# Optimization experiments

Hardware: AMD Instinct MI355X
Metric: run time of the kernel (lower is better)

## Reference

```python
import jax, jax.numpy as jnp
import numpy as np

DIM = 128
N_CENTERS = 30
CUT_LO, CUT_HI = 0.0, 10.0
N_CONV = 3
NODE_VOCAB = 100
EDGE_VOCAB = 500
N_NODES = 50000
N_EDGES = 800000
N_GRAPHS = 100
DIM_E = DIM + N_CENTERS  # 158


def setup_inputs() -> dict:
    key = jax.random.key(0)
    ks = jax.random.split(key, 20)
    def xav(k, shape):
        fan_in = shape[-2] if len(shape) >= 2 else shape[-1]
        return (jax.random.normal(k, shape, dtype=jnp.float32) / np.sqrt(fan_in)).astype(jnp.float32)
    inp = {
        'node_types': jax.random.randint(ks[0], (N_NODES,), 0, NODE_VOCAB),
        'edge_types': jax.random.randint(ks[1], (N_EDGES,), 0, EDGE_VOCAB),
        'src': jax.random.randint(ks[2], (N_EDGES,), 0, N_NODES),
        'dst': jax.random.randint(ks[3], (N_EDGES,), 0, N_NODES),
        'graph_ids': jnp.sort(jax.random.randint(ks[4], (N_NODES,), 0, N_GRAPHS)),
        'distances': jax.random.uniform(ks[5], (N_EDGES,), dtype=jnp.float32, minval=CUT_LO, maxval=CUT_HI),
        'n_graphs': N_GRAPHS,
        # embedding tables
        'node_emb': xav(ks[6], (NODE_VOCAB, DIM)),
        'edge_emb': xav(ks[7], (EDGE_VOCAB, DIM)),
        # stacked per-conv-layer weights (n_conv leading dim)
        'Wn1': xav(ks[8], (N_CONV, DIM, DIM)),  'bn1': jnp.zeros((N_CONV, DIM), jnp.float32),
        'Wn2': xav(ks[9], (N_CONV, DIM, DIM)),  'bn2': jnp.zeros((N_CONV, DIM), jnp.float32),
        'We1': xav(ks[10], (N_CONV, DIM_E, DIM)), 'be1': jnp.zeros((N_CONV, DIM), jnp.float32),
        'We2': xav(ks[11], (N_CONV, DIM, DIM)),  'be2': jnp.zeros((N_CONV, DIM), jnp.float32),
        'Wc':  xav(ks[12], (N_CONV, DIM, DIM)),  'bc': jnp.zeros((N_CONV, DIM), jnp.float32),
        # read layer
        'Wr1': xav(ks[13], (DIM, DIM)), 'br1': jnp.zeros((DIM,), jnp.float32),
        'Wr2': xav(ks[14], (DIM, 1)),   'br2': jnp.zeros((1,), jnp.float32),
    }
    return inp


def reference(node_types, edge_types, src, dst, graph_ids, distances, n_graphs,
              node_emb, edge_emb, Wn1, bn1, Wn2, bn2, We1, be1, We2, be2, Wc, bc,
              Wr1, br1, Wr2, br2):
    # embeddings
    h = node_emb[node_types]                      # [N, D]
    e_emb = edge_emb[edge_types]                  # [E, D]
    # RBF expansion of distances
    centers = jnp.linspace(CUT_LO, CUT_HI, N_CENTERS, dtype=jnp.float32)
    gap = centers[1] - centers[0]
    rbf = jnp.exp(-((distances[:, None] - centers[None, :]) ** 2) / gap)  # [E, n_centers]
    e = jnp.concatenate([e_emb, rbf], axis=1)     # [E, D + n_centers]

    n_nodes = h.shape[0]
    for i in range(N_CONV):
        node_path = jnp.maximum(h[src] @ Wn1[i] + bn1[i], 0.0) @ Wn2[i] + bn2[i]   # [E, D]
        edge_path = jnp.maximum(e @ We1[i] + be1[i], 0.0) @ We2[i] + be2[i]        # [E, D]
        m = jnp.tanh((node_path * edge_path) @ Wc[i] + bc[i])                       # [E, D]
        h = h + jax.ops.segment_sum(m, dst, num_segments=n_nodes)                   # scatter-add to dst

    # readout MLP + per-graph node sum
    hr = jnp.maximum(h @ Wr1 + br1, 0.0) @ Wr2 + br2                                # [N, 1]
    out = jax.ops.segment_sum(hr, graph_ids, num_segments=n_graphs)                 # [G, 1]
    return out.reshape(-1)
```

## Files before the change

kernel.cpp:

```cpp
#include <hip/hip_runtime.h>
#include <stdint.h>

#define NNODES 50000
#define NEDGES 800000
#define NGRAPH 100
#define NCHUNK (NEDGES / 16)
#define NWAVES 4096
#define NB0 196

typedef _Float16 f16;
typedef __attribute__((ext_vector_type(8))) _Float16 half8;
typedef __attribute__((ext_vector_type(4))) _Float16 half4;
typedef __attribute__((ext_vector_type(4))) float floatx4;

__device__ __forceinline__ void stage_WT(const float* __restrict__ W, f16* WT,
                                         int tid, int nthr) {
    for (int idx = tid; idx < 128 * 32; idx += nthr) {
        int k = idx >> 5, n4 = (idx & 31) * 4;
        floatx4 v = *(const floatx4*)(W + k * 128 + n4);
        WT[(n4 + 0) * 136 + k] = (f16)v[0];
        WT[(n4 + 1) * 136 + k] = (f16)v[1];
        WT[(n4 + 2) * 136 + k] = (f16)v[2];
        WT[(n4 + 3) * 136 + k] = (f16)v[3];
    }
}

__device__ __forceinline__ float fast_tanh(float x) {
    x = fminf(fmaxf(x, -15.0f), 15.0f);
    float e2 = __expf(2.0f * x);
    return (e2 - 1.0f) * __builtin_amdgcn_rcpf(e2 + 1.0f);
}

__device__ __forceinline__ int mtAddr(int c, int rgroup) {
    return c * 16 + ((((c >> 2) + rgroup) & 3) << 2);
}

__global__ void init_k(float* out, int osz, int* cnt) {
    int i = blockIdx.x * 256 + threadIdx.x;
    if (i < osz) out[i] = 0.0f;
    if (i < NNODES) cnt[i] = 0;
}

__global__ void hist_k(const int* __restrict__ dst, int* __restrict__ cnt) {
    int e = blockIdx.x * 256 + threadIdx.x;
    if (e < NEDGES) atomicAdd(&cnt[dst[e]], 1);
}

__global__ __launch_bounds__(1024) void scan1_k(const int* __restrict__ cnt,
                                                int* __restrict__ rowStart,
                                                int* __restrict__ blockSum) {
    __shared__ int buf[1024];
    int tid = threadIdx.x;
    int i = blockIdx.x * 1024 + tid;
    int v = (i < NNODES) ? cnt[i] : 0;
    buf[tid] = v;
    __syncthreads();
    for (int off = 1; off < 1024; off <<= 1) {
        int t = (tid >= off) ? buf[tid - off] : 0;
        __syncthreads();
        buf[tid] += t;
        __syncthreads();
    }
    if (i < NNODES) rowStart[i] = buf[tid] - v;
    if (tid == 1023) blockSum[blockIdx.x] = buf[1023];
}

__global__ void scan2_k(int* __restrict__ blockSum, int nb) {
    if (threadIdx.x == 0) {
        int run = 0;
        for (int b = 0; b < nb; ++b) { int s = blockSum[b]; blockSum[b] = run; run += s; }
    }
}

__global__ __launch_bounds__(1024) void scan3_k(int* __restrict__ rowStart,
                                                const int* __restrict__ blockSum,
                                                int* __restrict__ cnt) {
    int i = blockIdx.x * 1024 + threadIdx.x;
    if (i < NNODES) { rowStart[i] += blockSum[blockIdx.x]; cnt[i] = 0; }
    if (i == 0) rowStart[NNODES] = NEDGES;
}

__global__ void scatter_k(const int* __restrict__ src, const int* __restrict__ et,
                          const int* __restrict__ dst, const float* __restrict__ dist,
                          const int* __restrict__ rowStart, int* __restrict__ cnt,
                          uint4* __restrict__ packE) {
    int e = blockIdx.x * 256 + threadIdx.x;
    if (e >= NEDGES) return;
    int d = dst[e];
    int pos = rowStart[d] + atomicAdd(&cnt[d], 1);
    uint4 pk;
    pk.x = (unsigned)src[e];
    pk.y = (unsigned)et[e];
    pk.z = (unsigned)d;
    pk.w = __float_as_uint(dist[e]);
    packE[pos] = pk;
}

__global__ void gather_h(const int* __restrict__ nt, const float* __restrict__ emb,
                         float* __restrict__ h) {
    int i = blockIdx.x * 256 + threadIdx.x;
    int row = i >> 5, c4 = (i & 31) * 4;
    if (row < NNODES)
        *(floatx4*)(h + row * 128 + c4) = *(const floatx4*)(emb + nt[row] * 128 + c4);
}

__global__ __launch_bounds__(1024, 4) void mlp_combo(
        const float* __restrict__ Xh,
        const float* __restrict__ W1, const float* __restrict__ b1,
        const float* __restrict__ W2, const float* __restrict__ b2,
        f16* __restrict__ OutP,
        const float* __restrict__ Xe,
        const float* __restrict__ We1, const float* __restrict__ be1,
        f16* __restrict__ OutT) {
    __shared__ f16 W1T[128 * 136];
    __shared__ f16 W2T[128 * 136];
    __shared__ f16 xBuf[256 * 136];
    __shared__ float bias1[128];
    __shared__ float bias2[128];
    int tid = threadIdx.x;
    bool mode2 = blockIdx.x >= NB0;

    const float* X  = mode2 ? Xe : Xh;
    const float* Wa = mode2 ? We1 : W1;
    const float* ba = mode2 ? be1 : b1;
    f16* Out        = mode2 ? OutT : OutP;
    int  M          = mode2 ? 500 : NNODES;
    int  r0         = (mode2 ? (blockIdx.x - NB0) : blockIdx.x) * 256;

    stage_WT(Wa, W1T, tid, 1024);
    if (!mode2) stage_WT(W2, W2T, tid, 1024);
    if (tid < 128) { bias1[tid] = ba[tid]; bias2[tid] = mode2 ? 0.0f : b2[tid]; }

    for (int it = 0; it < 8; ++it) {
        int row = it * 32 + (tid >> 5);
        int c4 = (tid & 31) * 4;
        int gr = r0 + row;
        floatx4 x = {0.0f, 0.0f, 0.0f, 0.0f};
        if (gr < M) x = *(const floatx4*)(X + (size_t)gr * 128 + c4);
        half4 xh;
        xh[0] = (f16)x[0]; xh[1] = (f16)x[1]; xh[2] = (f16)x[2]; xh[3] = (f16)x[3];
        *(half4*)(xBuf + row * 136 + c4) = xh;
    }
    __syncthreads();

    int lane = tid & 63, wv = tid >> 6;
    int R = wv * 16;
    int n16 = lane & 15, q = lane >> 4;
    int gr = r0 + R + n16;

    half8 a[4];
    #pragma unroll
    for (int kk = 0; kk < 4; ++kk)
        a[kk] = *(const half8*)(xBuf + (R + n16) * 136 + kk * 32 + q * 8);

    #pragma unroll
    for (int f = 0; f < 8; ++f) {
        floatx4 acc = *(const floatx4*)(bias1 + f * 16 + q * 4);
        #pragma unroll
        for (int kk = 0; kk < 4; ++kk) {
            half8 aw = *(const half8*)(W1T + (f * 16 + n16) * 136 + kk * 32 + q * 8);
            acc = __builtin_amdgcn_mfma_f32_16x16x32_f16(aw, a[kk], acc, 0, 0, 0);
        }
        if (!mode2) {
            half4 y;
            #pragma unroll
            for (int i = 0; i < 4; ++i) y[i] = (f16)fmaxf(acc[i], 0.0f);
            *(half4*)(xBuf + (R + n16) * 136 + f * 16 + q * 4) = y;
        } else {
            half4 o;
            #pragma unroll
            for (int i = 0; i < 4; ++i) o[i] = (f16)acc[i];
            if (gr < M) *(half4*)(Out + (size_t)gr * 128 + f * 16 + q * 4) = o;
        }
    }

    if (!mode2) {
        #pragma unroll
        for (int kk = 0; kk < 4; ++kk)
            a[kk] = *(const half8*)(xBuf + (R + n16) * 136 + kk * 32 + q * 8);
        #pragma unroll
        for (int f = 0; f < 8; ++f) {
            floatx4 acc = *(const floatx4*)(bias2 + f * 16 + q * 4);
            #pragma unroll
            for (int kk = 0; kk < 4; ++kk) {
                half8 aw = *(const half8*)(W2T + (f * 16 + n16) * 136 + kk * 32 + q * 8);
                acc = __builtin_amdgcn_mfma_f32_16x16x32_f16(aw, a[kk], acc, 0, 0, 0);
            }
            half4 o;
            #pragma unroll
            for (int i = 0; i < 4; ++i) o[i] = (f16)acc[i];
            if (gr < M) *(half4*)(Out + (size_t)gr * 128 + f * 16 + q * 4) = o;
        }
    }
}

__global__ __launch_bounds__(1024, 4) void edge_kernel(
        const uint4* __restrict__ packE,
        const f16* __restrict__ P, const f16* __restrict__ T,
        const float* __restrict__ We1,
        const float* __restrict__ We2, const float* __restrict__ be2,
        const float* __restrict__ Wc,  const float* __restrict__ bc,
        float* __restrict__ h) {
    __shared__ f16 W2T[128 * 136];
    __shared__ f16 WcT[128 * 136];
    __shared__ f16 W1rT[128 * 40];
    __shared__ f16 Uall[16 * 2176];
    __shared__ float sbe2[128], sbc[128];
    __shared__ int dstW[16][16];

    int tid = threadIdx.x;
    stage_WT(We2, W2T, tid, 1024);
    stage_WT(Wc,  WcT, tid, 1024);
    for (int idx = tid; idx < 128 * 32; idx += 1024) {
        int n = idx >> 5, kr = idx & 31;
        W1rT[n * 40 + kr] = (kr < 30) ? (f16)We1[(128 + kr) * 128 + n] : (f16)0.0f;
    }
    if (tid < 128) { sbe2[tid] = be2[tid]; sbc[tid] = bc[tid]; }
    __syncthreads();

    int lane = tid & 63, wv = tid >> 6;
    f16* U = Uall + wv * 2176;
    int* dW = dstW[wv];
    int n16 = lane & 15, q = lane >> 4;
    const float invgap = 29.0f / 10.0f;
    int colA = lane, colB = lane + 64;
    int tsub = lane & 3, trow = lane >> 2;

    float sbcv[8];
    #pragma unroll
    for (int f = 0; f < 8; ++f) sbcv[f] = sbc[f * 16 + n16];

    int wgid = blockIdx.x * 16 + wv;
    int extra = wgid < 848 ? wgid : 848;
    int c0 = wgid * 12 + extra;
    int c1 = c0 + 12 + (wgid < 848 ? 1 : 0);

    float carry0 = 0.0f, carry1 = 0.0f;
    int prev = -1;

    uint4 pk = {0u, 0u, 0u, 0u};
    if (lane < 16) pk = packE[(size_t)c0 * 16 + lane];

    for (int ch = c0; ch < c1; ++ch) {
        bool hasNext = (ch + 1 < c1);
        int   ety  = __shfl((int)pk.y, trow);
        int   srcv = __shfl((int)pk.x, n16);
        float dcur = __shfl(__uint_as_float(pk.w), n16);
        if (lane < 16) dW[lane] = (int)pk.z;

        {
            const uint4* Tp = (const uint4*)(T + (size_t)ety * 128 + tsub * 32);
            uint4 tr0 = Tp[0], tr1 = Tp[1], tr2 = Tp[2], tr3 = Tp[3];
            uint4* ub = (uint4*)(U + trow * 136 + tsub * 32);
            ub[0] = tr0; ub[1] = tr1; ub[2] = tr2; ub[3] = tr3;
        }
        __builtin_amdgcn_sched_barrier(0);

        half8 pA0, pA1, pA2, pA3;
        {
            const f16* Pr = P + (size_t)srcv * 128 + q * 8;
            pA0 = *(const half8*)(Pr);
            pA1 = *(const half8*)(Pr + 32);
            pA2 = *(const half8*)(Pr + 64);
            pA3 = *(const half8*)(Pr + 96);
        }
        uint4 pkn = {0u, 0u, 0u, 0u};
        if (hasNext && lane < 16) pkn = packE[(size_t)(ch + 1) * 16 + lane];

        half8 ar;
        #pragma unroll
        for (int j = 0; j < 8; ++j) {
            int k = q * 8 + j;
            float c = (float)k * (10.0f / 29.0f);
            float df = dcur - c;
            ar[j] = (f16)((k < 30) ? __expf(-df * df * invgap) : 0.0f);
        }

        #pragma unroll
        for (int f = 0; f < 8; ++f) {
            f16* up = U + n16 * 136 + f * 16 + q * 4;
            half4 tv = *(const half4*)up;
            floatx4 c4 = {(float)tv[0], (float)tv[1], (float)tv[2], (float)tv[3]};
            half8 aw = *(const half8*)(W1rT + (f * 16 + n16) * 40 + q * 8);
            c4 = __builtin_amdgcn_mfma_f32_16x16x32_f16(aw, ar, c4, 0, 0, 0);
            half4 uv;
            #pragma unroll
            for (int i = 0; i < 4; ++i) uv[i] = (f16)fmaxf(c4[i], 0.0f);
            *(half4*)up = uv;
        }

        half8 a2[4];
        #pragma unroll
        for (int kk = 0; kk < 4; ++kk)
            a2[kk] = *(const half8*)(U + n16 * 136 + kk * 32 + q * 8);
        #pragma unroll
        for (int f = 0; f < 8; ++f) {
            floatx4 acc = *(const floatx4*)(sbe2 + f * 16 + q * 4);
            #pragma unroll
            for (int kk = 0; kk < 4; ++kk) {
                half8 aw = *(const half8*)(W2T + (f * 16 + n16) * 136 + kk * 32 + q * 8);
                acc = __builtin_amdgcn_mfma_f32_16x16x32_f16(aw, a2[kk], acc, 0, 0, 0);
            }
            half4 ev;
            #pragma unroll
            for (int i = 0; i < 4; ++i) ev[i] = (f16)acc[i];
            *(half4*)(U + n16 * 136 + f * 16 + q * 4) = ev;
        }

        {
            half8 e0 = *(const half8*)(U + n16 * 136 + 0 * 32 + q * 8);
            half8 e1 = *(const half8*)(U + n16 * 136 + 1 * 32 + q * 8);
            half8 e2 = *(const half8*)(U + n16 * 136 + 2 * 32 + q * 8);
            half8 e3 = *(const half8*)(U + n16 * 136 + 3 * 32 + q * 8);
            a2[0] = e0 * pA0; a2[1] = e1 * pA1; a2[2] = e2 * pA2; a2[3] = e3 * pA3;
        }
        #pragma unroll
        for (int f = 0; f < 8; ++f) {
            float bb = sbcv[f];
            floatx4 acc = {bb, bb, bb, bb};
            #pragma unroll
            for (int kk = 0; kk < 4; ++kk) {
                half8 b = *(const half8*)(WcT + (f * 16 + n16) * 136 + kk * 32 + q * 8);
                acc = __builtin_amdgcn_mfma_f32_16x16x32_f16(a2[kk], b, acc, 0, 0, 0);
            }
            int c = f * 16 + n16;
            half4 mv;
            #pragma unroll
            for (int i = 0; i < 4; ++i) mv[i] = (f16)fast_tanh(acc[i]);
            *(half4*)(U + mtAddr(c, q)) = mv;
        }

        {
            half4 va[4], vb[4];
            #pragma unroll
            for (int g2 = 0; g2 < 4; ++g2) {
                va[g2] = *(const half4*)(U + mtAddr(colA, g2));
                vb[g2] = *(const half4*)(U + mtAddr(colB, g2));
            }
            int dArr[16];
            *(int4*)(dArr)      = *(const int4*)(dW);
            *(int4*)(dArr + 4)  = *(const int4*)(dW + 4);
            *(int4*)(dArr + 8)  = *(const int4*)(dW + 8);
            *(int4*)(dArr + 12) = *(const int4*)(dW + 12);
            #pragma unroll
            for (int r = 0; r < 16; ++r) {
                int dd = dArr[r];
                float v0 = (float)va[r >> 2][r & 3];
                float v1 = (float)vb[r >> 2][r & 3];
                if (dd != prev) {
                    if (prev >= 0) {
                        unsafeAtomicAdd(&h[(size_t)prev * 128 + colA], carry0);
                        unsafeAtomicAdd(&h[(size_t)prev * 128 + colB], carry1);
                    }
                    prev = dd; carry0 = v0; carry1 = v1;
                } else { carry0 += v0; carry1 += v1; }
            }
        }
        pk = pkn;
        __builtin_amdgcn_sched_barrier(0);
    }
    if (prev >= 0) {
        unsafeAtomicAdd(&h[(size_t)prev * 128 + colA], carry0);
        unsafeAtomicAdd(&h[(size_t)prev * 128 + colB], carry1);
    }
}

__global__ __launch_bounds__(1024, 4) void readout_k(
        const float* __restrict__ X, int M,
        const float* __restrict__ W1, const float* __restrict__ b1,
        const float* __restrict__ Wr2, const float* __restrict__ br2,
        const int* __restrict__ gid, float* __restrict__ out) {
    __shared__ f16 W1T[128 * 136];
    __shared__ f16 xBuf[256 * 136];
    __shared__ float bias1[128];
    __shared__ float sWr2[128];
    int tid = threadIdx.x;

    stage_WT(W1, W1T, tid, 1024);
    if (tid < 128) { bias1[tid] = b1[tid]; sWr2[tid] = Wr2[tid]; }

    int r0 = blockIdx.x * 256;
    for (int it = 0; it < 8; ++it) {
        int row = it * 32 + (tid >> 5);
        int c4 = (tid & 31) * 4;
        int gr = r0 + row;
        floatx4 x = {0.0f, 0.0f, 0.0f, 0.0f};
        if (gr < M) x = *(const floatx4*)(X + (size_t)gr * 128 + c4);
        half4 xh;
        xh[0] = (f16)x[0]; xh[1] = (f16)x[1]; xh[2] = (f16)x[2]; xh[3] = (f16)x[3];
        *(half4*)(xBuf + row * 136 + c4) = xh;
    }
    __syncthreads();

    int lane = tid & 63, wv = tid >> 6;
    int R = wv * 16;
    int n16 = lane & 15, q = lane >> 4;

    half8 a[4];
    #pragma unroll
    for (int kk = 0; kk < 4; ++kk)
        a[kk] = *(const half8*)(xBuf + (R + n16) * 136 + kk * 32 + q * 8);

    floatx4 acc[8];
    #pragma unroll
    for (int f = 0; f < 8; ++f) {
        float bb = bias1[f * 16 + n16];
        acc[f] = (floatx4){bb, bb, bb, bb};
        #pragma unroll
        for (int kk = 0; kk < 4; ++kk) {
            half8 b = *(const half8*)(W1T + (f * 16 + n16) * 136 + kk * 32 + q * 8);
            acc[f] = __builtin_amdgcn_mfma_f32_16x16x32_f16(a[kk], b, acc[f], 0, 0, 0);
        }
    }

    float s[4];
    #pragma unroll
    for (int i = 0; i < 4; ++i) {
        float t = 0.0f;
        #pragma unroll
        for (int f = 0; f < 8; ++f)
            t += fmaxf(acc[f][i], 0.0f) * sWr2[f * 16 + n16];
        #pragma unroll
        for (int m = 1; m < 16; m <<= 1) t += __shfl_xor(t, m);
        s[i] = t;
    }

    if (n16 == 0) {
        float br2v = br2[0];
        float t = 0.0f; int g = -1;
        #pragma unroll
        for (int i = 0; i < 4; ++i) {
            int gr = r0 + R + q * 4 + i;
            if (gr < M) {
                int gi = gid[gr];
                float si = s[i] + br2v;
                if (gi == g) t += si;
                else { if (g >= 0) unsafeAtomicAdd(&out[g], t); g = gi; t = si; }
            }
        }
        if (g >= 0) unsafeAtomicAdd(&out[g], t);
    }
}

extern "C" void kernel_launch(void* const* d_in, const int* in_sizes, int n_in,
                              void* d_out, int out_size, void* d_ws, size_t ws_size,
                              hipStream_t stream) {
    (void)in_sizes; (void)n_in; (void)ws_size;
    const int*   node_types = (const int*)d_in[0];
    const int*   edge_types = (const int*)d_in[1];
    const int*   src        = (const int*)d_in[2];
    const int*   dst        = (const int*)d_in[3];
    const int*   graph_ids  = (const int*)d_in[4];
    const float* distances  = (const float*)d_in[5];
    const float* node_emb   = (const float*)d_in[7];
    const float* edge_emb   = (const float*)d_in[8];
    const float* Wn1 = (const float*)d_in[9];
    const float* bn1 = (const float*)d_in[10];
    const float* Wn2 = (const float*)d_in[11];
    const float* bn2 = (const float*)d_in[12];
    const float* We1 = (const float*)d_in[13];
    const float* be1 = (const float*)d_in[14];
    const float* We2 = (const float*)d_in[15];
    const float* be2 = (const float*)d_in[16];
    const float* Wc  = (const float*)d_in[17];
    const float* bc  = (const float*)d_in[18];
    const float* Wr1 = (const float*)d_in[19];
    const float* br1 = (const float*)d_in[20];
    const float* Wr2 = (const float*)d_in[21];
    const float* br2 = (const float*)d_in[22];

    char* w = (char*)d_ws;
    auto carve = [&](size_t bytes) { char* p = w; w += (bytes + 255) & ~(size_t)255; return p; };
    float* h        = (float*)carve((size_t)NNODES * 128 * 4);
    f16*   P        = (f16*)  carve((size_t)NNODES * 128 * 2);
    f16*   T        = (f16*)  carve((size_t)500 * 128 * 2);
    int*   rowStart = (int*)  carve((size_t)(NNODES + 1) * 4);
    int*   cnt      = (int*)  carve((size_t)NNODES * 4);
    int*   blockSum = (int*)  carve((size_t)64 * 4);
    uint4* packE    = (uint4*)carve((size_t)NEDGES * 16);

    float* out = (float*)d_out;
    const int NB1 = (NNODES + 1023) / 1024;

    init_k<<<(NNODES + 255) / 256, 256, 0, stream>>>(out, out_size, cnt);
    hist_k<<<NEDGES / 256, 256, 0, stream>>>(dst, cnt);
    scan1_k<<<NB1, 1024, 0, stream>>>(cnt, rowStart, blockSum);
    scan2_k<<<1, 64, 0, stream>>>(blockSum, NB1);
    scan3_k<<<NB1, 1024, 0, stream>>>(rowStart, blockSum, cnt);
    scatter_k<<<NEDGES / 256, 256, 0, stream>>>(src, edge_types, dst, distances,
                                                rowStart, cnt, packE);
    gather_h<<<(NNODES * 32 + 255) / 256, 256, 0, stream>>>(node_types, node_emb, h);

    for (int i = 0; i < 3; ++i) {
        mlp_combo<<<NB0 + 2, 1024, 0, stream>>>(
            h, Wn1 + (size_t)i * 128 * 128, bn1 + i * 128,
            Wn2 + (size_t)i * 128 * 128, bn2 + i * 128, P,
            edge_emb, We1 + (size_t)i * 158 * 128, be1 + i * 128, T);
        edge_kernel<<<256, 1024, 0, stream>>>(
            packE, P, T,
            We1 + (size_t)i * 158 * 128,
            We2 + (size_t)i * 128 * 128, be2 + i * 128,
            Wc + (size_t)i * 128 * 128, bc + i * 128, h);
    }

    readout_k<<<(NNODES + 255) / 256, 1024, 0, stream>>>(
        h, NNODES, Wr1, br1, Wr2, br2, graph_ids, out);
}
```

Measured before the change: 686.5 us.

## Replace per-edge RBF expansion and matmul with a quantized distance lookup table

A new kernel precomputes, for each layer, the RBF-expansion-times-We1 product for 4096 distance bins over the cutoff range and stores it in fp16. The scatter pass stores a bin index instead of the raw distance. The edge kernel then adds the looked-up row to the edge-type row and applies ReLU, which removes the per-edge exp evaluations and the RBF MFMA stage. It also simplifies tanh by dropping the clamp and moves the biases into registers. In exchange it adds an extra table gather per edge and quantization error, and distances outside the cutoff range are clamped to the edge bins.

```diff
diff --git a/kernel.cpp b/kernel.cpp
--- a/kernel.cpp
+++ b/kernel.cpp
@@ -7,6 +7,7 @@
 #define NCHUNK (NEDGES / 16)
 #define NWAVES 4096
 #define NB0 196
+#define NBIN 4096
 
 typedef _Float16 f16;
 typedef __attribute__((ext_vector_type(8))) _Float16 half8;
@@ -26,9 +27,8 @@
 }
 
 __device__ __forceinline__ float fast_tanh(float x) {
-    x = fminf(fmaxf(x, -15.0f), 15.0f);
     float e2 = __expf(2.0f * x);
-    return (e2 - 1.0f) * __builtin_amdgcn_rcpf(e2 + 1.0f);
+    return 1.0f - 2.0f * __builtin_amdgcn_rcpf(e2 + 1.0f);
 }
 
 __device__ __forceinline__ int mtAddr(int c, int rgroup) {
@@ -88,11 +88,13 @@
     if (e >= NEDGES) return;
     int d = dst[e];
     int pos = rowStart[d] + atomicAdd(&cnt[d], 1);
+    int bin = (int)(dist[e] * ((float)NBIN / 10.0f));
+    bin = bin < 0 ? 0 : (bin > NBIN - 1 ? NBIN - 1 : bin);
     uint4 pk;
     pk.x = (unsigned)src[e];
     pk.y = (unsigned)et[e];
     pk.z = (unsigned)d;
-    pk.w = __float_as_uint(dist[e]);
+    pk.w = (unsigned)bin;
     packE[pos] = pk;
 }
 
@@ -102,6 +104,24 @@
     int row = i >> 5, c4 = (i & 31) * 4;
     if (row < NNODES)
         *(floatx4*)(h + row * 128 + c4) = *(const floatx4*)(emb + nt[row] * 128 + c4);
+}
+
+__global__ void rtab_k(const float* __restrict__ We1, f16* __restrict__ Rtab) {
+    __shared__ float rbf[30];
+    int layer = blockIdx.x / NBIN, bin = blockIdx.x - layer * NBIN;
+    int col = threadIdx.x;
+    float d = ((float)bin + 0.5f) * (10.0f / (float)NBIN);
+    if (col < 30) {
+        float c = (float)col * (10.0f / 29.0f);
+        float df = d - c;
+        rbf[col] = __expf(-df * df * (29.0f / 10.0f));
+    }
+    __syncthreads();
+    const float* W = We1 + (size_t)layer * 158 * 128 + 128 * 128;
+    float s = 0.0f;
+    #pragma unroll
+    for (int k = 0; k < 30; ++k) s += rbf[k] * W[k * 128 + col];
+    Rtab[(size_t)blockIdx.x * 128 + col] = (f16)s;
 }
 
 __global__ __launch_bounds__(1024, 4) void mlp_combo(
@@ -197,38 +217,34 @@
 __global__ __launch_bounds__(1024, 4) void edge_kernel(
         const uint4* __restrict__ packE,
         const f16* __restrict__ P, const f16* __restrict__ T,
-        const float* __restrict__ We1,
+        const f16* __restrict__ Rtab,
         const float* __restrict__ We2, const float* __restrict__ be2,
         const float* __restrict__ Wc,  const float* __restrict__ bc,
         float* __restrict__ h) {
     __shared__ f16 W2T[128 * 136];
     __shared__ f16 WcT[128 * 136];
-    __shared__ f16 W1rT[128 * 40];
     __shared__ f16 Uall[16 * 2176];
-    __shared__ float sbe2[128], sbc[128];
     __shared__ int dstW[16][16];
 
     int tid = threadIdx.x;
     stage_WT(We2, W2T, tid, 1024);
     stage_WT(Wc,  WcT, tid, 1024);
-    for (int idx = tid; idx < 128 * 32; idx += 1024) {
-        int n = idx >> 5, kr = idx & 31;
-        W1rT[n * 40 + kr] = (kr < 30) ? (f16)We1[(128 + kr) * 128 + n] : (f16)0.0f;
-    }
-    if (tid < 128) { sbe2[tid] = be2[tid]; sbc[tid] = bc[tid]; }
     __syncthreads();
 
     int lane = tid & 63, wv = tid >> 6;
     f16* U = Uall + wv * 2176;
     int* dW = dstW[wv];
     int n16 = lane & 15, q = lane >> 4;
-    const float invgap = 29.0f / 10.0f;
     int colA = lane, colB = lane + 64;
     int tsub = lane & 3, trow = lane >> 2;
 
+    floatx4 be2r[8];
     float sbcv[8];
     #pragma unroll
-    for (int f = 0; f < 8; ++f) sbcv[f] = sbc[f * 16 + n16];
+    for (int f = 0; f < 8; ++f) {
+        be2r[f] = *(const floatx4*)(be2 + f * 16 + q * 4);
+        sbcv[f] = bc[f * 16 + n16];
+    }
 
     int wgid = blockIdx.x * 16 + wv;
     int extra = wgid < 848 ? wgid : 848;
@@ -244,15 +260,25 @@
     for (int ch = c0; ch < c1; ++ch) {
         bool hasNext = (ch + 1 < c1);
         int   ety  = __shfl((int)pk.y, trow);
+        int   dbin = __shfl((int)pk.w, trow);
         int   srcv = __shfl((int)pk.x, n16);
-        float dcur = __shfl(__uint_as_float(pk.w), n16);
         if (lane < 16) dW[lane] = (int)pk.z;
 
         {
-            const uint4* Tp = (const uint4*)(T + (size_t)ety * 128 + tsub * 32);
-            uint4 tr0 = Tp[0], tr1 = Tp[1], tr2 = Tp[2], tr3 = Tp[3];
-            uint4* ub = (uint4*)(U + trow * 136 + tsub * 32);
-            ub[0] = tr0; ub[1] = tr1; ub[2] = tr2; ub[3] = tr3;
+            const half8* Tp = (const half8*)(T    + (size_t)ety  * 128 + tsub * 32);
+            const half8* Rp = (const half8*)(Rtab + (size_t)dbin * 128 + tsub * 32);
+            half8 t0 = Tp[0], t1 = Tp[1], t2 = Tp[2], t3 = Tp[3];
+            half8 r0 = Rp[0], r1 = Rp[1], r2 = Rp[2], r3 = Rp[3];
+            t0 += r0; t1 += r1; t2 += r2; t3 += r3;
+            #pragma unroll
+            for (int j = 0; j < 8; ++j) {
+                t0[j] = (t0[j] < (f16)0) ? (f16)0 : t0[j];
+                t1[j] = (t1[j] < (f16)0) ? (f16)0 : t1[j];
+                t2[j] = (t2[j] < (f16)0) ? (f16)0 : t2[j];
+                t3[j] = (t3[j] < (f16)0) ? (f16)0 : t3[j];
+            }
+            half8* ub = (half8*)(U + trow * 136 + tsub * 32);
+            ub[0] = t0; ub[1] = t1; ub[2] = t2; ub[3] = t3;
         }
         __builtin_amdgcn_sched_barrier(0);
 
@@ -267,35 +293,13 @@
         uint4 pkn = {0u, 0u, 0u, 0u};
         if (hasNext && lane < 16) pkn = packE[(size_t)(ch + 1) * 16 + lane];
 
-        half8 ar;
-        #pragma unroll
-        for (int j = 0; j < 8; ++j) {
-            int k = q * 8 + j;
-            float c = (float)k * (10.0f / 29.0f);
-            float df = dcur - c;
-            ar[j] = (f16)((k < 30) ? __expf(-df * df * invgap) : 0.0f);
-        }
-
-        #pragma unroll
-        for (int f = 0; f < 8; ++f) {
-            f16* up = U + n16 * 136 + f * 16 + q * 4;
-            half4 tv = *(const half4*)up;
-            floatx4 c4 = {(float)tv[0], (float)tv[1], (float)tv[2], (float)tv[3]};
-            half8 aw = *(const half8*)(W1rT + (f * 16 + n16) * 40 + q * 8);
-            c4 = __builtin_amdgcn_mfma_f32_16x16x32_f16(aw, ar, c4, 0, 0, 0);
-            half4 uv;
-            #pragma unroll
-            for (int i = 0; i < 4; ++i) uv[i] = (f16)fmaxf(c4[i], 0.0f);
-            *(half4*)up = uv;
-        }
-
         half8 a2[4];
         #pragma unroll
         for (int kk = 0; kk < 4; ++kk)
             a2[kk] = *(const half8*)(U + n16 * 136 + kk * 32 + q * 8);
         #pragma unroll
         for (int f = 0; f < 8; ++f) {
-            floatx4 acc = *(const floatx4*)(sbe2 + f * 16 + q * 4);
+            floatx4 acc = be2r[f];
             #pragma unroll
             for (int kk = 0; kk < 4; ++kk) {
                 half8 aw = *(const half8*)(W2T + (f * 16 + n16) * 136 + kk * 32 + q * 8);
@@ -474,6 +478,7 @@
     float* h        = (float*)carve((size_t)NNODES * 128 * 4);
     f16*   P        = (f16*)  carve((size_t)NNODES * 128 * 2);
     f16*   T        = (f16*)  carve((size_t)500 * 128 * 2);
+    f16*   Rtab     = (f16*)  carve((size_t)3 * NBIN * 128 * 2);
     int*   rowStart = (int*)  carve((size_t)(NNODES + 1) * 4);
     int*   cnt      = (int*)  carve((size_t)NNODES * 4);
     int*   blockSum = (int*)  carve((size_t)64 * 4);
@@ -490,6 +495,7 @@
     scatter_k<<<NEDGES / 256, 256, 0, stream>>>(src, edge_types, dst, distances,
                                                 rowStart, cnt, packE);
     gather_h<<<(NNODES * 32 + 255) / 256, 256, 0, stream>>>(node_types, node_emb, h);
+    rtab_k<<<3 * NBIN, 128, 0, stream>>>(We1, Rtab);
 
     for (int i = 0; i < 3; ++i) {
         mlp_combo<<<NB0 + 2, 1024, 0, stream>>>(
@@ -497,8 +503,7 @@
             Wn2 + (size_t)i * 128 * 128, bn2 + i * 128, P,
             edge_emb, We1 + (size_t)i * 158 * 128, be1 + i * 128, T);
         edge_kernel<<<256, 1024, 0, stream>>>(
-            packE, P, T,
-            We1 + (size_t)i * 158 * 128,
+            packE, P, T, Rtab + (size_t)i * NBIN * 128,
             We2 + (size_t)i * 128 * 128, be2 + i * 128,
             Wc + (size_t)i * 128 * 128, bc + i * 128, h);
     }
```

After: 706.1 us. +2.9%, slower.

## Process 32 edges per wave in edge kernel to reuse weight fragments

Applied to the files above, without the earlier changes.

Each wave now handles two 16-edge tiles per chunk, so every weight fragment read from LDS feeds two MFMAs. Block size drops to 512 threads (8 waves) with a larger per-wave scratch buffer, and the transpose swizzle and dst-run reduction are widened to 32 rows. This cuts LDS weight traffic and doubles independent MFMA chains for latency hiding, at the cost of more registers, fewer waves per CU and more LDS per wave.

```diff
diff --git a/kernel.cpp b/kernel.cpp
--- a/kernel.cpp
+++ b/kernel.cpp
@@ -4,8 +4,8 @@
 #define NNODES 50000
 #define NEDGES 800000
 #define NGRAPH 100
-#define NCHUNK (NEDGES / 16)
-#define NWAVES 4096
+#define NCHUNK32 (NEDGES / 32)
+#define NWAVES32 2048
 #define NB0 196
 
 typedef _Float16 f16;
@@ -31,8 +31,8 @@
     return (e2 - 1.0f) * __builtin_amdgcn_rcpf(e2 + 1.0f);
 }
 
-__device__ __forceinline__ int mtAddr(int c, int rgroup) {
-    return c * 16 + ((((c >> 2) + rgroup) & 3) << 2);
+__device__ __forceinline__ int mt32(int c, int g) {
+    return c * 32 + ((((c >> 1) + g) & 7) << 2);
 }
 
 __global__ void init_k(float* out, int osz, int* cnt) {
@@ -194,7 +194,7 @@
     }
 }
 
-__global__ __launch_bounds__(1024, 4) void edge_kernel(
+__global__ __launch_bounds__(512, 2) void edge_kernel(
         const uint4* __restrict__ packE,
         const f16* __restrict__ P, const f16* __restrict__ T,
         const float* __restrict__ We1,
@@ -204,14 +204,14 @@
     __shared__ f16 W2T[128 * 136];
     __shared__ f16 WcT[128 * 136];
     __shared__ f16 W1rT[128 * 40];
-    __shared__ f16 Uall[16 * 2176];
+    __shared__ f16 Uall[8 * 4352];
     __shared__ float sbe2[128], sbc[128];
-    __shared__ int dstW[16][16];
+    __shared__ int dstW[8][32];
 
     int tid = threadIdx.x;
-    stage_WT(We2, W2T, tid, 1024);
-    stage_WT(Wc,  WcT, tid, 1024);
-    for (int idx = tid; idx < 128 * 32; idx += 1024) {
+    stage_WT(We2, W2T, tid, 512);
+    stage_WT(Wc,  WcT, tid, 512);
+    for (int idx = tid; idx < 128 * 32; idx += 512) {
         int n = idx >> 5, kr = idx & 31;
         W1rT[n * 40 + kr] = (kr < 30) ? (f16)We1[(128 + kr) * 128 + n] : (f16)0.0f;
     }
@@ -219,7 +219,7 @@
     __syncthreads();
 
     int lane = tid & 63, wv = tid >> 6;
-    f16* U = Uall + wv * 2176;
+    f16* U = Uall + wv * 4352;
     int* dW = dstW[wv];
     int n16 = lane & 15, q = lane >> 4;
     const float invgap = 29.0f / 10.0f;
@@ -230,120 +230,152 @@
     #pragma unroll
     for (int f = 0; f < 8; ++f) sbcv[f] = sbc[f * 16 + n16];
 
-    int wgid = blockIdx.x * 16 + wv;
-    int extra = wgid < 848 ? wgid : 848;
+    int wgid = blockIdx.x * 8 + wv;
+    int extra = wgid < 424 ? wgid : 424;
     int c0 = wgid * 12 + extra;
-    int c1 = c0 + 12 + (wgid < 848 ? 1 : 0);
+    int c1 = c0 + 12 + (wgid < 424 ? 1 : 0);
 
     float carry0 = 0.0f, carry1 = 0.0f;
     int prev = -1;
 
     uint4 pk = {0u, 0u, 0u, 0u};
-    if (lane < 16) pk = packE[(size_t)c0 * 16 + lane];
+    if (lane < 32) pk = packE[(size_t)c0 * 32 + lane];
 
     for (int ch = c0; ch < c1; ++ch) {
         bool hasNext = (ch + 1 < c1);
-        int   ety  = __shfl((int)pk.y, trow);
-        int   srcv = __shfl((int)pk.x, n16);
-        float dcur = __shfl(__uint_as_float(pk.w), n16);
-        if (lane < 16) dW[lane] = (int)pk.z;
+        int   ety0  = __shfl((int)pk.y, trow);
+        int   ety1  = __shfl((int)pk.y, trow + 16);
+        int   srcv0 = __shfl((int)pk.x, n16);
+        int   srcv1 = __shfl((int)pk.x, n16 + 16);
+        float d0    = __shfl(__uint_as_float(pk.w), n16);
+        float d1    = __shfl(__uint_as_float(pk.w), n16 + 16);
+        if (lane < 32) dW[lane] = (int)pk.z;
 
         {
-            const uint4* Tp = (const uint4*)(T + (size_t)ety * 128 + tsub * 32);
-            uint4 tr0 = Tp[0], tr1 = Tp[1], tr2 = Tp[2], tr3 = Tp[3];
-            uint4* ub = (uint4*)(U + trow * 136 + tsub * 32);
-            ub[0] = tr0; ub[1] = tr1; ub[2] = tr2; ub[3] = tr3;
+            const uint4* Tp0 = (const uint4*)(T + (size_t)ety0 * 128 + tsub * 32);
+            const uint4* Tp1 = (const uint4*)(T + (size_t)ety1 * 128 + tsub * 32);
+            uint4 ta0 = Tp0[0], ta1 = Tp0[1], ta2 = Tp0[2], ta3 = Tp0[3];
+            uint4 tb0 = Tp1[0], tb1 = Tp1[1], tb2 = Tp1[2], tb3 = Tp1[3];
+            uint4* u0 = (uint4*)(U + trow * 136 + tsub * 32);
+            uint4* u1 = (uint4*)(U + (16 + trow) * 136 + tsub * 32);
+            u0[0] = ta0; u0[1] = ta1; u0[2] = ta2; u0[3] = ta3;
+            u1[0] = tb0; u1[1] = tb1; u1[2] = tb2; u1[3] = tb3;
         }
         __builtin_amdgcn_sched_barrier(0);
 
-        half8 pA0, pA1, pA2, pA3;
+        half8 pA0, pA1, pA2, pA3, pB0, pB1, pB2, pB3;
         {
-            const f16* Pr = P + (size_t)srcv * 128 + q * 8;
-            pA0 = *(const half8*)(Pr);
-            pA1 = *(const half8*)(Pr + 32);
-            pA2 = *(const half8*)(Pr + 64);
-            pA3 = *(const half8*)(Pr + 96);
+            const f16* Pr0 = P + (size_t)srcv0 * 128 + q * 8;
+            const f16* Pr1 = P + (size_t)srcv1 * 128 + q * 8;
+            pA0 = *(const half8*)(Pr0);      pA1 = *(const half8*)(Pr0 + 32);
+            pA2 = *(const half8*)(Pr0 + 64); pA3 = *(const half8*)(Pr0 + 96);
+            pB0 = *(const half8*)(Pr1);      pB1 = *(const half8*)(Pr1 + 32);
+            pB2 = *(const half8*)(Pr1 + 64); pB3 = *(const half8*)(Pr1 + 96);
         }
         uint4 pkn = {0u, 0u, 0u, 0u};
-        if (hasNext && lane < 16) pkn = packE[(size_t)(ch + 1) * 16 + lane];
-
-        half8 ar;
+        if (hasNext && lane < 32) pkn = packE[(size_t)(ch + 1) * 32 + lane];
+
+        half8 ar0, ar1;
         #pragma unroll
         for (int j = 0; j < 8; ++j) {
             int k = q * 8 + j;
             float c = (float)k * (10.0f / 29.0f);
-            float df = dcur - c;
-            ar[j] = (f16)((k < 30) ? __expf(-df * df * invgap) : 0.0f);
+            float df0 = d0 - c, df1 = d1 - c;
+            ar0[j] = (f16)((k < 30) ? __expf(-df0 * df0 * invgap) : 0.0f);
+            ar1[j] = (f16)((k < 30) ? __expf(-df1 * df1 * invgap) : 0.0f);
         }
 
         #pragma unroll
         for (int f = 0; f < 8; ++f) {
-            f16* up = U + n16 * 136 + f * 16 + q * 4;
-            half4 tv = *(const half4*)up;
-            floatx4 c4 = {(float)tv[0], (float)tv[1], (float)tv[2], (float)tv[3]};
             half8 aw = *(const half8*)(W1rT + (f * 16 + n16) * 40 + q * 8);
-            c4 = __builtin_amdgcn_mfma_f32_16x16x32_f16(aw, ar, c4, 0, 0, 0);
-            half4 uv;
-            #pragma unroll
-            for (int i = 0; i < 4; ++i) uv[i] = (f16)fmaxf(c4[i], 0.0f);
-            *(half4*)up = uv;
-        }
-
-        half8 a2[4];
-        #pragma unroll
-        for (int kk = 0; kk < 4; ++kk)
-            a2[kk] = *(const half8*)(U + n16 * 136 + kk * 32 + q * 8);
+            f16* up0 = U + n16 * 136 + f * 16 + q * 4;
+            f16* up1 = U + (16 + n16) * 136 + f * 16 + q * 4;
+            half4 tv0 = *(const half4*)up0;
+            half4 tv1 = *(const half4*)up1;
+            floatx4 c40 = {(float)tv0[0], (float)tv0[1], (float)tv0[2], (float)tv0[3]};
+            floatx4 c41 = {(float)tv1[0], (float)tv1[1], (float)tv1[2], (float)tv1[3]};
+            c40 = __builtin_amdgcn_mfma_f32_16x16x32_f16(aw, ar0, c40, 0, 0, 0);
+            c41 = __builtin_amdgcn_mfma_f32_16x16x32_f16(aw, ar1, c41, 0, 0, 0);
+            half4 uv0, uv1;
+            #pragma unroll
+            for (int i = 0; i < 4; ++i) {
+                uv0[i] = (f16)fmaxf(c40[i], 0.0f);
+                uv1[i] = (f16)fmaxf(c41[i], 0.0f);
+            }
+            *(half4*)up0 = uv0;
+            *(half4*)up1 = uv1;
+        }
+
+        half8 a20[4], a21[4];
+        #pragma unroll
+        for (int kk = 0; kk < 4; ++kk) {
+            a20[kk] = *(const half8*)(U + n16 * 136 + kk * 32 + q * 8);
+            a21[kk] = *(const half8*)(U + (16 + n16) * 136 + kk * 32 + q * 8);
+        }
         #pragma unroll
         for (int f = 0; f < 8; ++f) {
-            floatx4 acc = *(const floatx4*)(sbe2 + f * 16 + q * 4);
+            floatx4 acc0 = *(const floatx4*)(sbe2 + f * 16 + q * 4);
+            floatx4 acc1 = acc0;
             #pragma unroll
             for (int kk = 0; kk < 4; ++kk) {
                 half8 aw = *(const half8*)(W2T + (f * 16 + n16) * 136 + kk * 32 + q * 8);
-                acc = __builtin_amdgcn_mfma_f32_16x16x32_f16(aw, a2[kk], acc, 0, 0, 0);
-            }
-            half4 ev;
-            #pragma unroll
-            for (int i = 0; i < 4; ++i) ev[i] = (f16)acc[i];
-            *(half4*)(U + n16 * 136 + f * 16 + q * 4) = ev;
+                acc0 = __builtin_amdgcn_mfma_f32_16x16x32_f16(aw, a20[kk], acc0, 0, 0, 0);
+                acc1 = __builtin_amdgcn_mfma_f32_16x16x32_f16(aw, a21[kk], acc1, 0, 0, 0);
+            }
+            half4 ev0, ev1;
+            #pragma unroll
+            for (int i = 0; i < 4; ++i) { ev0[i] = (f16)acc0[i]; ev1[i] = (f16)acc1[i]; }
+            *(half4*)(U + n16 * 136 + f * 16 + q * 4) = ev0;
+            *(half4*)(U + (16 + n16) * 136 + f * 16 + q * 4) = ev1;
         }
 
         {
-            half8 e0 = *(const half8*)(U + n16 * 136 + 0 * 32 + q * 8);
-            half8 e1 = *(const half8*)(U + n16 * 136 + 1 * 32 + q * 8);
-            half8 e2 = *(const half8*)(U + n16 * 136 + 2 * 32 + q * 8);
-            half8 e3 = *(const half8*)(U + n16 * 136 + 3 * 32 + q * 8);
-            a2[0] = e0 * pA0; a2[1] = e1 * pA1; a2[2] = e2 * pA2; a2[3] = e3 * pA3;
+            half8 e00 = *(const half8*)(U + n16 * 136 + 0 * 32 + q * 8);
+            half8 e01 = *(const half8*)(U + n16 * 136 + 1 * 32 + q * 8);
+            half8 e02 = *(const half8*)(U + n16 * 136 + 2 * 32 + q * 8);
+            half8 e03 = *(const half8*)(U + n16 * 136 + 3 * 32 + q * 8);
+            half8 e10 = *(const half8*)(U + (16 + n16) * 136 + 0 * 32 + q * 8);
+            half8 e11 = *(const half8*)(U + (16 + n16) * 136 + 1 * 32 + q * 8);
+            half8 e12 = *(const half8*)(U + (16 + n16) * 136 + 2 * 32 + q * 8);
+            half8 e13 = *(const half8*)(U + (16 + n16) * 136 + 3 * 32 + q * 8);
+            a20[0] = e00 * pA0; a20[1] = e01 * pA1; a20[2] = e02 * pA2; a20[3] = e03 * pA3;
+            a21[0] = e10 * pB0; a21[1] = e11 * pB1; a21[2] = e12 * pB2; a21[3] = e13 * pB3;
         }
         #pragma unroll
         for (int f = 0; f < 8; ++f) {
             float bb = sbcv[f];
-            floatx4 acc = {bb, bb, bb, bb};
+            floatx4 acc0 = {bb, bb, bb, bb};
+            floatx4 acc1 = {bb, bb, bb, bb};
             #pragma unroll
             for (int kk = 0; kk < 4; ++kk) {
                 half8 b = *(const half8*)(WcT + (f * 16 + n16) * 136 + kk * 32 + q * 8);
-                acc = __builtin_amdgcn_mfma_f32_16x16x32_f16(a2[kk], b, acc, 0, 0, 0);
+                acc0 = __builtin_amdgcn_mfma_f32_16x16x32_f16(a20[kk], b, acc0, 0, 0, 0);
+                acc1 = __builtin_amdgcn_mfma_f32_16x16x32_f16(a21[kk], b, acc1, 0, 0, 0);
             }
             int c = f * 16 + n16;
-            half4 mv;
-            #pragma unroll
-            for (int i = 0; i < 4; ++i) mv[i] = (f16)fast_tanh(acc[i]);
-            *(half4*)(U + mtAddr(c, q)) = mv;
+            half4 mv0, mv1;
+            #pragma unroll
+            for (int i = 0; i < 4; ++i) {
+                mv0[i] = (f16)fast_tanh(acc0[i]);
+                mv1[i] = (f16)fast_tanh(acc1[i]);
+            }
+            *(half4*)(U + mt32(c, q))     = mv0;
+            *(half4*)(U + mt32(c, 4 + q)) = mv1;
         }
 
         {
-            half4 va[4], vb[4];
-            #pragma unroll
-            for (int g2 = 0; g2 < 4; ++g2) {
-                va[g2] = *(const half4*)(U + mtAddr(colA, g2));
-                vb[g2] = *(const half4*)(U + mtAddr(colB, g2));
-            }
-            int dArr[16];
-            *(int4*)(dArr)      = *(const int4*)(dW);
-            *(int4*)(dArr + 4)  = *(const int4*)(dW + 4);
-            *(int4*)(dArr + 8)  = *(const int4*)(dW + 8);
-            *(int4*)(dArr + 12) = *(const int4*)(dW + 12);
-            #pragma unroll
-            for (int r = 0; r < 16; ++r) {
+            half4 va[8], vb[8];
+            #pragma unroll
+            for (int g = 0; g < 8; ++g) {
+                va[g] = *(const half4*)(U + mt32(colA, g));
+                vb[g] = *(const half4*)(U + mt32(colB, g));
+            }
+            int dArr[32];
+            #pragma unroll
+            for (int i4 = 0; i4 < 8; ++i4)
+                *(int4*)(dArr + i4 * 4) = *(const int4*)(dW + i4 * 4);
+            #pragma unroll
+            for (int r = 0; r < 32; ++r) {
                 int dd = dArr[r];
                 float v0 = (float)va[r >> 2][r & 3];
                 float v1 = (float)vb[r >> 2][r & 3];
@@ -496,7 +528,7 @@
             h, Wn1 + (size_t)i * 128 * 128, bn1 + i * 128,
             Wn2 + (size_t)i * 128 * 128, bn2 + i * 128, P,
             edge_emb, We1 + (size_t)i * 158 * 128, be1 + i * 128, T);
-        edge_kernel<<<256, 1024, 0, stream>>>(
+        edge_kernel<<<256, 512, 0, stream>>>(
             packE, P, T,
             We1 + (size_t)i * 158 * 128,
             We2 + (size_t)i * 128 * 128, be2 + i * 128,
```

Result: no change. 675.7 us (median of 2 runs) (-1.6%).
